# Performance work log

Hardware: AMD Instinct MI355X
Metric: run time of the kernel (lower is better)

Reference implementation:

```python
import jax, jax.numpy as jnp
import numpy as np

N_LAYERS = 2
D = 128


def _prelu(z, a):
    return jnp.where(z >= 0, z, a * z)


def _seg_sum(vals, idx, num):
    return jax.ops.segment_sum(vals, idx, num_segments=num)


def _conv_layer(x, ni, ei, Wn2e, bn2e, We2n, be2n, alpha, Dn_inv, De_inv, num_nodes, num_edges):
    # node -> edge: mean over member nodes (row norm), then linear + bias + PReLU
    e = _seg_sum((x @ Wn2e)[ni] * De_inv[ei][:, None], ei, num_edges) + bn2e
    e = _prelu(e, alpha)
    # edge -> node: mean over incident hyperedges
    n = _seg_sum((e @ We2n)[ei] * Dn_inv[ni][:, None], ni, num_nodes) + be2n
    return n, e


def _encoder(x, ni, ei, Wn2e, bn2e, We2n, be2n, alpha, Dn_inv, De_inv, num_nodes, num_edges):
    e = None
    for i in range(N_LAYERS):
        x, e = _conv_layer(x, ni, ei, Wn2e[i], bn2e[i], We2n[i], be2n[i], alpha, Dn_inv, De_inv, num_nodes, num_edges)
        x = _prelu(x, alpha)
    return x, e


def _decoder(x, e, ni, ei, We, Wx, b, alpha, Dn_inv, num_nodes):
    for i in range(N_LAYERS):
        m = _seg_sum((e @ We[i])[ei] * Dn_inv[ni][:, None], ni, num_nodes)
        x = _prelu(x @ Wx[i] + m + b[i], alpha)
    return x


def _forward(x, xx,
             e1_Wn2e, e1_bn2e, e1_We2n, e1_be2n,
             e2_Wn2e, e2_bn2e, e2_We2n, e2_be2n,
             d1_We, d1_Wx, d1_b, d2_We, d2_Wx, d2_b,
             alpha, node_idx, edge_idx, num_nodes, num_edges):
    # self loops: each node gets its own private hyperedge (id num_edges + node_id)
    ni = jnp.concatenate([node_idx, jnp.arange(num_nodes, dtype=node_idx.dtype)])
    ei = jnp.concatenate([edge_idx, jnp.arange(num_edges, num_edges + num_nodes, dtype=edge_idx.dtype)])
    ne_tot = num_edges + num_nodes
    ones = jnp.ones(ni.shape[0], x.dtype)
    Dn = _seg_sum(ones, ni, num_nodes)
    De = _seg_sum(ones, ei, ne_tot)
    Dn_inv = jnp.where(Dn > 0, 1.0 / Dn, 0.0)
    De_inv = jnp.where(De > 0, 1.0 / De, 0.0)

    n1, e1 = _encoder(x, ni, ei, e1_Wn2e, e1_bn2e, e1_We2n, e1_be2n, alpha, Dn_inv, De_inv, num_nodes, ne_tot)
    n2, e2 = _encoder(xx, ni, ei, e2_Wn2e, e2_bn2e, e2_We2n, e2_be2n, alpha, Dn_inv, De_inv, num_nodes, ne_tot)

    x11 = _decoder(n1, e1, ni, ei, d1_We, d1_Wx, d1_b, alpha, Dn_inv, num_nodes)
    x21 = _decoder(n2, e2, ni, ei, d2_We, d2_Wx, d2_b, alpha, Dn_inv, num_nodes)
    x12 = _decoder(n2, e2, ni, ei, d1_We, d1_Wx, d1_b, alpha, Dn_inv, num_nodes)
    x22 = _decoder(n1, e1, ni, ei, d2_We, d2_Wx, d2_b, alpha, Dn_inv, num_nodes)

    nn1 = jnp.concatenate([n1, n2], axis=1)
    return (nn1, n1, e1[:num_edges], n2, e2[:num_edges], x11, x21, x12, x22)


def setup_inputs() -> dict:
    key = jax.random.key(0)
    ks = jax.random.split(key, 24)
    N, E, NNZ = 50000, 20000, 800000
    s = 1.0 / np.sqrt(D)
    inp = {
        'x': jax.random.normal(ks[0], (N, D), jnp.float32),
        'xx': jax.random.normal(ks[1], (N, D), jnp.float32),
        'node_idx': jax.random.randint(ks[2], (NNZ,), 0, N, jnp.int32),
        'edge_idx': jax.random.randint(ks[3], (NNZ,), 0, E, jnp.int32),
        'num_nodes': N,
        'num_edges': E,
        'alpha': jnp.float32(0.25),
    }
    i = 4
    for enc in ('e1', 'e2'):
        inp[enc + '_Wn2e'] = jax.random.normal(ks[i], (N_LAYERS, D, D), jnp.float32) * s; i += 1
        inp[enc + '_bn2e'] = jnp.zeros((N_LAYERS, D), jnp.float32)
        inp[enc + '_We2n'] = jax.random.normal(ks[i], (N_LAYERS, D, D), jnp.float32) * s; i += 1
        inp[enc + '_be2n'] = jnp.zeros((N_LAYERS, D), jnp.float32)
    for dec in ('d1', 'd2'):
        inp[dec + '_We'] = jax.random.normal(ks[i], (N_LAYERS, D, D), jnp.float32) * s; i += 1
        inp[dec + '_Wx'] = jax.random.normal(ks[i], (N_LAYERS, D, D), jnp.float32) * s; i += 1
        inp[dec + '_b'] = jnp.zeros((N_LAYERS, D), jnp.float32)
    return inp


def reference(x, xx,
              e1_Wn2e, e1_bn2e, e1_We2n, e1_be2n,
              e2_Wn2e, e2_bn2e, e2_We2n, e2_be2n,
              d1_We, d1_Wx, d1_b, d2_We, d2_Wx, d2_b,
              alpha, node_idx, edge_idx, num_nodes, num_edges):
    return _forward(x, xx,
                    e1_Wn2e, e1_bn2e, e1_We2n, e1_be2n,
                    e2_Wn2e, e2_bn2e, e2_We2n, e2_be2n,
                    d1_We, d1_Wx, d1_b, d2_We, d2_Wx, d2_b,
                    alpha, node_idx, edge_idx, num_nodes, num_edges)
```

## Files before the change

### kernel.cpp

```cpp
#include <hip/hip_runtime.h>

#define DD 128

typedef __attribute__((ext_vector_type(8))) short bh8;
typedef __attribute__((ext_vector_type(8))) unsigned short us8;
typedef __attribute__((ext_vector_type(4))) unsigned short us4;
typedef __attribute__((ext_vector_type(4))) float f4;
typedef unsigned int u32;
typedef unsigned short u16;

__device__ __forceinline__ u16 tob(float f) {
  u32 u = __builtin_bit_cast(u32, f);
  u += 0x7FFFu + ((u >> 16) & 1u);
  return (u16)(u >> 16);
}
__device__ __forceinline__ float fb(u16 h) { return __builtin_bit_cast(float, (u32)h << 16); }


__global__ __launch_bounds__(256) void init_counts_k(int* cn, int* ce, int N, int E) {
  int g = blockIdx.x * blockDim.x + threadIdx.x;
  if (g < E) ce[g] = 0;
  if (g < N) cn[g] = 0;
}

__global__ __launch_bounds__(256) void hist_k(const int* __restrict__ ni, const int* __restrict__ ei,
                                              int* cn, int* ce, int nnz) {
  int stride = gridDim.x * blockDim.x;
  for (int j = blockIdx.x * blockDim.x + threadIdx.x; j < nnz; j += stride) {
    atomicAdd(&cn[ni[j]], 1);
    atomicAdd(&ce[ei[j]], 1);
  }
}

__global__ __launch_bounds__(1024) void exscan2_k(const int* __restrict__ cn, int* offs_n, int N,
                                                  const int* __restrict__ ce, int* offs_e, int E) {
  const int* cnt = blockIdx.x ? ce : cn;
  int* offs = blockIdx.x ? offs_e : offs_n;
  int n = blockIdx.x ? E : N;
  __shared__ int sums[1024];
  __shared__ int carry;
  const int tid = threadIdx.x;
  if (tid == 0) carry = 0;
  __syncthreads();
  const int PER = 8;
  const int CH = 1024 * PER;
  for (int base = 0; base < n; base += CH) {
    int i0 = base + tid * PER;
    int v[PER]; int s = 0;
    #pragma unroll
    for (int j = 0; j < PER; ++j) { int i = i0 + j; int t = (i < n) ? cnt[i] : 0; v[j] = t; s += t; }
    sums[tid] = s;
    __syncthreads();
    for (int off = 1; off < 1024; off <<= 1) {
      int t = (tid >= off) ? sums[tid - off] : 0;
      __syncthreads();
      sums[tid] += t;
      __syncthreads();
    }
    int excl = sums[tid] - s + carry;
    #pragma unroll
    for (int j = 0; j < PER; ++j) { int i = i0 + j; if (i < n) offs[i] = excl; excl += v[j]; }
    __syncthreads();
    if (tid == 0) carry += sums[1023];
    __syncthreads();
  }
  if (tid == 0) offs[n] = carry;
}

__global__ __launch_bounds__(256) void fill_deg_k(const int* __restrict__ offs_n, const int* __restrict__ offs_e,
                                                  float* Dn_inv, float* De_inv,
                                                  int* cur_be, int* cur_bn, int* cur_n, int* cur_e,
                                                  int N, int E, int NBE, int NBN) {
  int g = blockIdx.x * blockDim.x + threadIdx.x;
  if (g < E) {
    int b = offs_e[g], e = offs_e[g + 1];
    De_inv[g] = (e > b) ? 1.0f / (float)(e - b) : 0.0f;
    cur_e[g] = b;
  }
  if (g < N) {
    int b = offs_n[g], e = offs_n[g + 1];
    Dn_inv[g] = 1.0f / (float)(e - b + 1);
    cur_n[g] = b;
  }
  if (g < NBE) {
    int r1 = (g + 1) * 32; if (r1 > E) r1 = E;
    int o0 = offs_e[g * 32], o1 = offs_e[r1];
    int C = o1 - o0, base = 8 * o0;
    #pragma unroll
    for (int k = 0; k < 8; ++k) cur_be[g * 8 + k] = base + k * C;
  }
  if (g < NBN) {
    int r1 = (g + 1) * 32; if (r1 > N) r1 = N;
    int o0 = offs_n[g * 32], o1 = offs_n[r1];
    int C = o1 - o0, base = 8 * o0;
    #pragma unroll
    for (int k = 0; k < 8; ++k) cur_bn[g * 8 + k] = base + k * C;
  }
}

__global__ __launch_bounds__(256) void partition2_k(const int* __restrict__ ni, const int* __restrict__ ei,
                                                    int* cur_be, int* cur_bn,
                                                    u32* __restrict__ SE, u32* __restrict__ SN, int nnz) {
  int xcd;
  asm volatile("s_getreg_b32 %0, hwreg(HW_REG_XCC_ID)" : "=s"(xcd));
  xcd &= 7;
  int stride = gridDim.x * blockDim.x;
  for (int j = blockIdx.x * blockDim.x + threadIdx.x; j < nnz; j += stride) {
    int n = ni[j], e = ei[j];
    int pe = atomicAdd(&cur_be[(e >> 5) * 8 + xcd], 1);
    SE[pe] = ((u32)(e & 31) << 17) | (u32)n;
    int pn = atomicAdd(&cur_bn[(n >> 5) * 8 + xcd], 1);
    SN[pn] = ((u32)(n & 31) << 17) | (u32)e;
  }
}

__global__ __launch_bounds__(256) void scatter2_k(const u32* __restrict__ S, const int* __restrict__ offs,
                                                  const int* __restrict__ cur_b,
                                                  int* __restrict__ list, int nRows) {
  __shared__ int cur[32];
  const int b = blockIdx.x;
  const int i0 = b << 5;
  const int tid = threadIdx.x;
  if (tid < 32) {
    int row = i0 + tid;
    cur[tid] = (row < nRows) ? offs[row] : 0;
  }
  __syncthreads();
  int r1 = i0 + 32; if (r1 > nRows) r1 = nRows;
  const int o0 = offs[i0];
  const int C = offs[r1] - o0;
  #pragma unroll 1
  for (int k = 0; k < 8; ++k) {
    int sbeg = 8 * o0 + k * C;
    int send = cur_b[b * 8 + k];
    for (int i = sbeg + tid; i < send; i += 256) {
      u32 v = S[i];
      int pos = atomicAdd(&cur[v >> 17], 1);
      list[pos] = (int)(v & 0x1FFFFu);
    }
  }
}

__global__ __launch_bounds__(256) void fill_nnz_k(const int* __restrict__ ni, const int* __restrict__ ei,
                                                  int* cur_n, int* cur_e, int* listN, int* listE, int nnz) {
  int stride = gridDim.x * blockDim.x;
  for (int j = blockIdx.x * blockDim.x + threadIdx.x; j < nnz; j += stride) {
    int n = ni[j], e = ei[j];
    int pn = atomicAdd(&cur_n[n], 1); listN[pn] = e;
    int pe = atomicAdd(&cur_e[e], 1); listE[pe] = n;
  }
}


__device__ __forceinline__ void acc4(float4& a, us4 v) {
  a.x += fb(v[0]); a.y += fb(v[1]); a.z += fb(v[2]); a.w += fb(v[3]);
}

template<int SPLIT>
__global__ __launch_bounds__(256) void gather_edge_k(const u16* __restrict__ srcb,
                                                     const int* __restrict__ offs, const int* __restrict__ list,
                                                     const float* __restrict__ De_inv,
                                                     const float* __restrict__ b1, const float* __restrict__ b2,
                                                     const float* __restrict__ alphap,
                                                     u16* __restrict__ e_fullb,
                                                     float* __restrict__ d2a, float* __restrict__ d2b, int E) {
  const int wave = threadIdx.x >> 6, lane = threadIdx.x & 63;
  const int row = blockIdx.x * 4 + wave;
  if (row >= E) return;
  const int c = lane * 4;
  const int beg = offs[row], end = offs[row + 1];
  float4 a0 = {0,0,0,0}, a1 = {0,0,0,0}, a2 = {0,0,0,0}, a3 = {0,0,0,0};
  int i = beg;
  for (; i + 3 < end; i += 4) {
    int s0 = list[i], s1 = list[i + 1], s2 = list[i + 2], s3 = list[i + 3];
    us4 v0 = *(const us4*)&srcb[(size_t)s0 * 256 + c];
    us4 v1 = *(const us4*)&srcb[(size_t)s1 * 256 + c];
    us4 v2 = *(const us4*)&srcb[(size_t)s2 * 256 + c];
    us4 v3 = *(const us4*)&srcb[(size_t)s3 * 256 + c];
    acc4(a0, v0); acc4(a1, v1); acc4(a2, v2); acc4(a3, v3);
  }
  for (; i < end; ++i) acc4(a0, *(const us4*)&srcb[(size_t)list[i] * 256 + c]);
  float sc = De_inv[row];
  const float* bp = (c < 128) ? (b1 + c) : (b2 + c - 128);
  float4 bt = *(const float4*)bp;
  float al = *alphap;
  float4 o;
  o.x = sc * ((a0.x + a1.x) + (a2.x + a3.x)) + bt.x;
  o.y = sc * ((a0.y + a1.y) + (a2.y + a3.y)) + bt.y;
  o.z = sc * ((a0.z + a1.z) + (a2.z + a3.z)) + bt.z;
  o.w = sc * ((a0.w + a1.w) + (a2.w + a3.w)) + bt.w;
  o.x = (o.x >= 0.f) ? o.x : al * o.x;
  o.y = (o.y >= 0.f) ? o.y : al * o.y;
  o.z = (o.z >= 0.f) ? o.z : al * o.z;
  o.w = (o.w >= 0.f) ? o.w : al * o.w;
  us4 ob = {tob(o.x), tob(o.y), tob(o.z), tob(o.w)};
  *(us4*)&e_fullb[(size_t)row * 256 + c] = ob;
  if constexpr (SPLIT == 1) {
    if (c < 128) *(float4*)&d2a[(size_t)row * DD + c] = o;
    else         *(float4*)&d2b[(size_t)row * DD + c - 128] = o;
  }
}

__global__ __launch_bounds__(256) void gather_node_k(const u16* __restrict__ e_fullb,
                                                     const u16* __restrict__ tb,
                                                     const int* __restrict__ offs, const int* __restrict__ list,
                                                     const float* __restrict__ Dn_inv,
                                                     const float* __restrict__ b1, const float* __restrict__ b2,
                                                     const float* __restrict__ alphap,
                                                     u16* __restrict__ dstb, int N) {
  const int wave = threadIdx.x >> 6, lane = threadIdx.x & 63;
  const int row = blockIdx.x * 4 + wave;
  if (row >= N) return;
  const int c = lane * 4;
  const int beg = offs[row], end = offs[row + 1];
  float4 a0 = {0,0,0,0}, a1 = {0,0,0,0}, a2 = {0,0,0,0}, a3 = {0,0,0,0};
  int i = beg;
  for (; i + 3 < end; i += 4) {
    int s0 = list[i], s1 = list[i + 1], s2 = list[i + 2], s3 = list[i + 3];
    us4 v0 = *(const us4*)&e_fullb[(size_t)s0 * 256 + c];
    us4 v1 = *(const us4*)&e_fullb[(size_t)s1 * 256 + c];
    us4 v2 = *(const us4*)&e_fullb[(size_t)s2 * 256 + c];
    us4 v3 = *(const us4*)&e_fullb[(size_t)s3 * 256 + c];
    acc4(a0, v0); acc4(a1, v1); acc4(a2, v2); acc4(a3, v3);
  }
  for (; i < end; ++i) acc4(a0, *(const us4*)&e_fullb[(size_t)list[i] * 256 + c]);
  us4 tv4 = *(const us4*)&tb[(size_t)row * 256 + c];
  const float* bp = (c < 128) ? (b1 + c) : (b2 + c - 128);
  float4 bt = *(const float4*)bp;
  float al = *alphap;
  float sx = fb(tv4[0]) + bt.x; sx = (sx >= 0.f) ? sx : al * sx;
  float sy = fb(tv4[1]) + bt.y; sy = (sy >= 0.f) ? sy : al * sy;
  float sz = fb(tv4[2]) + bt.z; sz = (sz >= 0.f) ? sz : al * sz;
  float sw = fb(tv4[3]) + bt.w; sw = (sw >= 0.f) ? sw : al * sw;
  float sc = Dn_inv[row];
  us4 ob;
  ob[0] = tob(sc * (sx + ((a0.x + a1.x) + (a2.x + a3.x))));
  ob[1] = tob(sc * (sy + ((a0.y + a1.y) + (a2.y + a3.y))));
  ob[2] = tob(sc * (sz + ((a0.z + a1.z) + (a2.z + a3.z))));
  ob[3] = tob(sc * (sw + ((a0.w + a1.w) + (a2.w + a3.w))));
  *(us4*)&dstb[(size_t)row * 256 + c] = ob;
}


struct WPtrs { const float* p[16]; };

__global__ __launch_bounds__(256) void prep_w_k(WPtrs wp, char* dst) {
  int m = blockIdx.x >> 3, s = blockIdx.x & 7;
  const float* W = wp.p[m];
  int t = threadIdx.x;
  int n = t & 127;
  int k0 = s * 16 + (t >> 7) * 8;
  us8 vhi, vlo;
  #pragma unroll
  for (int j = 0; j < 8; ++j) {
    float x = W[(size_t)(k0 + j) * DD + n];
    u32 ux = __builtin_bit_cast(u32, x);
    float hf = __builtin_bit_cast(float, ux & 0xFFFF0000u);
    float l = x - hf;
    vhi[j] = (u16)(ux >> 16);
    vlo[j] = (u16)(__builtin_bit_cast(u32, l) >> 16);
  }
  char* base = dst + (size_t)m * 65536;
  int byte = n * 256 + k0 * 2;
  byte ^= (n & 7) << 4;
  *(us8*)(base + byte) = vhi;
  *(us8*)(base + 32768 + byte) = vlo;
}


__device__ __forceinline__ void stage_w(const char* gsrc, char* lds, int tid) {
  int wave = tid >> 6, lane = tid & 63;
  #pragma unroll
  for (int i = 0; i < 16; ++i) {
    int off = (wave * 16 + i) * 1024;
    __builtin_amdgcn_global_load_lds(
        (const __attribute__((address_space(1))) u32*)(gsrc + off + lane * 16),
        (__attribute__((address_space(3))) u32*)(lds + off), 16, 0, 0);
  }
}

__device__ __forceinline__ void split8(const float vs[8], bh8& hi, bh8& lo) {
  #pragma unroll
  for (int j = 0; j < 8; ++j) {
    u32 u = __builtin_bit_cast(u32, vs[j]);
    float hf = __builtin_bit_cast(float, u & 0xFFFF0000u);
    float l = vs[j] - hf;
    hi[j] = (short)(u >> 16);
    lo[j] = (short)(__builtin_bit_cast(u32, l) >> 16);
  }
}

__device__ __forceinline__ void mk_afrag(const float* rowp, int koff, bh8& hi, bh8& lo) {
  float4 v0 = *(const float4*)(rowp + koff);
  float4 v1 = *(const float4*)(rowp + koff + 4);
  float vs[8] = {v0.x, v0.y, v0.z, v0.w, v1.x, v1.y, v1.z, v1.w};
  split8(vs, hi, lo);
}

__device__ __forceinline__ void mfma_ks(const bh8& ahi, const bh8& alo, const char* Wl,
                                        int ks, int lane, f4 acc[8]) {
  const int koff0 = (lane >> 4) * 8;
  const int k2 = (ks * 32 + koff0) * 2;
  #pragma unroll
  for (int cb = 0; cb < 8; ++cb) {
    int n = cb * 16 + (lane & 15);
    int byte = (n * 256 + k2) ^ ((n & 7) << 4);
    bh8 bhiF = *(const bh8*)(Wl + byte);
    bh8 bloF = *(const bh8*)(Wl + 32768 + byte);
    acc[cb] = __builtin_amdgcn_mfma_f32_16x16x32_bf16(ahi, bhiF, acc[cb], 0, 0, 0);
    acc[cb] = __builtin_amdgcn_mfma_f32_16x16x32_bf16(ahi, bloF, acc[cb], 0, 0, 0);
    acc[cb] = __builtin_amdgcn_mfma_f32_16x16x32_bf16(alo, bhiF, acc[cb], 0, 0, 0);
  }
}

__device__ __forceinline__ void mfma_ks_bf(const bh8& a, const char* Wl,
                                           int ks, int lane, f4 acc[8]) {
  const int koff0 = (lane >> 4) * 8;
  const int k2 = (ks * 32 + koff0) * 2;
  #pragma unroll
  for (int cb = 0; cb < 8; ++cb) {
    int n = cb * 16 + (lane & 15);
    int byte = (n * 256 + k2) ^ ((n & 7) << 4);
    bh8 bhiF = *(const bh8*)(Wl + byte);
    bh8 bloF = *(const bh8*)(Wl + 32768 + byte);
    acc[cb] = __builtin_amdgcn_mfma_f32_16x16x32_bf16(a, bhiF, acc[cb], 0, 0, 0);
    acc[cb] = __builtin_amdgcn_mfma_f32_16x16x32_bf16(a, bloF, acc[cb], 0, 0, 0);
  }
}

__device__ __forceinline__ void mfma_passS(const float* __restrict__ A, size_t astride, int acoff,
                                           const char* Wl, int rbase, int nrows, int lane, f4 acc[8]) {
  int r = rbase + (lane & 15);
  if (r >= nrows) r = nrows - 1;
  const float* rowp = A + (size_t)r * astride + acoff;
  const int koff0 = (lane >> 4) * 8;
  #pragma unroll
  for (int ks = 0; ks < 4; ++ks) {
    bh8 ahi, alo;
    mk_afrag(rowp, ks * 32 + koff0, ahi, alo);
    mfma_ks(ahi, alo, Wl, ks, lane, acc);
  }
}

__device__ __forceinline__ void mfma_passB(const u16* __restrict__ A, size_t astride, int acoff,
                                           const char* Wl, int rbase, int nrows, int lane, f4 acc[8]) {
  int r = rbase + (lane & 15);
  if (r >= nrows) r = nrows - 1;
  const u16* rowp = A + (size_t)r * astride + acoff;
  const int koff0 = (lane >> 4) * 8;
  #pragma unroll
  for (int ks = 0; ks < 4; ++ks) {
    bh8 a = __builtin_bit_cast(bh8, *(const us8*)(rowp + ks * 32 + koff0));
    mfma_ks_bf(a, Wl, ks, lane, acc);
  }
}

struct AFragB { bh8 a[4]; };

__device__ __forceinline__ void load_afragB(const u16* __restrict__ A, size_t astride, int acoff,
                                            int rbase, int nrows, int lane, AFragB& f) {
  int r = rbase + (lane & 15);
  if (r >= nrows) r = nrows - 1;
  const u16* rowp = A + (size_t)r * astride + acoff;
  const int koff0 = (lane >> 4) * 8;
  #pragma unroll
  for (int ks = 0; ks < 4; ++ks)
    f.a[ks] = __builtin_bit_cast(bh8, *(const us8*)(rowp + ks * 32 + koff0));
}

__device__ __forceinline__ void mfma_pass_fragB(const AFragB& f, const char* Wl, int lane, f4 acc[8]) {
  #pragma unroll
  for (int ks = 0; ks < 4; ++ks) mfma_ks_bf(f.a[ks], Wl, ks, lane, acc);
}

template<int MODE, int OBF>
__device__ __forceinline__ void epilogueS(f4 acc[8], const float* bias, const float* alphap,
                                          void* outp, size_t ostride, int ocoff,
                                          int rbase, int nrows, int lane) {
  float al = 0.f;
  if constexpr (MODE == 1) al = *alphap;
  const int cidx = lane & 15;
  int rq = rbase + (lane >> 4) * 4;
  float b8[8];
  if constexpr (MODE == 1) {
    #pragma unroll
    for (int cb = 0; cb < 8; ++cb) b8[cb] = bias[cb * 16 + cidx];
  }
  #pragma unroll
  for (int q = 0; q < 4; ++q) {
    int row = rq + q;
    if (row < nrows) {
      #pragma unroll
      for (int cb = 0; cb < 8; ++cb) {
        float v = acc[cb][q];
        if constexpr (MODE == 1) { v += b8[cb]; v = (v >= 0.f) ? v : al * v; }
        if constexpr (OBF == 1) {
          u16* op = (u16*)outp + (size_t)row * ostride + ocoff + cidx;
          op[cb * 16] = tob(v);
        } else {
          float* op = (float*)outp + (size_t)row * ostride + ocoff + cidx;
          op[cb * 16] = v;
        }
      }
    }
  }
}

#define ACC_ZERO(acc) { _Pragma("unroll") for (int cb = 0; cb < 8; ++cb) acc[cb] = {0.f, 0.f, 0.f, 0.f}; }


template<int MODE, int OBF, int ABF>
__global__ __launch_bounds__(256, 2) void gemm_halves_k(const void* __restrict__ A1, size_t as1, int ac1, const char* W1, const float* b1_,
                                                        const void* __restrict__ A2, size_t as2, int ac2, const char* W2, const float* b2_,
                                                        const float* __restrict__ alphap,
                                                        void* __restrict__ out, int nrows) {
  __shared__ char Wl[65536];
  const int wave = threadIdx.x >> 6, lane = threadIdx.x & 63;
  const int rbase = blockIdx.x * 64 + wave * 16;
  f4 acc[8];
  stage_w(W1, Wl, threadIdx.x);
  __syncthreads();
  ACC_ZERO(acc);
  if constexpr (ABF) mfma_passB((const u16*)A1, as1, ac1, Wl, rbase, nrows, lane, acc);
  else               mfma_passS((const float*)A1, as1, ac1, Wl, rbase, nrows, lane, acc);
  epilogueS<MODE, OBF>(acc, b1_, alphap, out, 256, 0, rbase, nrows, lane);
  __syncthreads();
  stage_w(W2, Wl, threadIdx.x);
  __syncthreads();
  ACC_ZERO(acc);
  if constexpr (ABF) mfma_passB((const u16*)A2, as2, ac2, Wl, rbase, nrows, lane, acc);
  else               mfma_passS((const float*)A2, as2, ac2, Wl, rbase, nrows, lane, acc);
  epilogueS<MODE, OBF>(acc, b2_, alphap, out, 256, 128, rbase, nrows, lane);
}

__global__ __launch_bounds__(256, 2) void enc_final_k(const u16* __restrict__ aggb, const char* W1, const float* b1_,
                                                      const char* W2, const float* b2_,
                                                      const float* __restrict__ alphap,
                                                      float* __restrict__ n1, float* __restrict__ n2,
                                                      u16* __restrict__ n1b, u16* __restrict__ n2b,
                                                      float* __restrict__ nn1, int nrows) {
  __shared__ char Wl[65536];
  const int wave = threadIdx.x >> 6, lane = threadIdx.x & 63;
  const int rbase = blockIdx.x * 64 + wave * 16;
  const int cidx = lane & 15;
  f4 acc[8];
  float al = *alphap;
  #pragma unroll 1
  for (int h = 0; h < 2; ++h) {
    if (h) __syncthreads();
    stage_w(h ? W2 : W1, Wl, threadIdx.x);
    __syncthreads();
    const float* bp = h ? b2_ : b1_;
    float* nout = h ? n2 : n1;
    u16* nbout = h ? n2b : n1b;
    float b8[8];
    #pragma unroll
    for (int cb = 0; cb < 8; ++cb) b8[cb] = bp[cb * 16 + cidx];
    ACC_ZERO(acc);
    mfma_passB(aggb, 256, h * 128, Wl, rbase, nrows, lane, acc);
    int rq = rbase + (lane >> 4) * 4;
    #pragma unroll
    for (int q = 0; q < 4; ++q) {
      int row = rq + q;
      if (row < nrows) {
        float* op = nout + (size_t)row * DD + cidx;
        float* op2 = nn1 + (size_t)row * 256 + h * 128 + cidx;
        u16* op3 = nbout + (size_t)row * DD + cidx;
        #pragma unroll
        for (int cb = 0; cb < 8; ++cb) {
          float v = acc[cb][q] + b8[cb];
          v = (v >= 0.f) ? v : al * v;
          op[cb * 16] = v;
          op2[cb * 16] = v;
          op3[cb * 16] = tob(v);
        }
      }
    }
  }
}

template<int OBF>
__global__ __launch_bounds__(256, 2) void dec_pair2b_k(const u16* __restrict__ xA0, const u16* __restrict__ xB0,
                                                       const u16* __restrict__ xA1, const u16* __restrict__ xB1,
                                                       const u16* __restrict__ aggb,
                                                       const char* WxA, const char* WeA, const float* bA,
                                                       const char* WxB, const char* WeB, const float* bB,
                                                       const float* __restrict__ alphap,
                                                       void* __restrict__ o1_0, void* __restrict__ o2_0,
                                                       void* __restrict__ o1_1, void* __restrict__ o2_1,
                                                       int nrows) {
  __shared__ char Wl[65536];
  const int y = blockIdx.y;
  const u16* xA = y ? xA1 : xA0;
  const u16* xB = y ? xB1 : xB0;
  void* o1 = y ? o1_1 : o1_0;
  void* o2 = y ? o2_1 : o2_0;
  const int acoff = y * 128;
  const int wave = threadIdx.x >> 6, lane = threadIdx.x & 63;
  const int rbase = blockIdx.x * 64 + wave * 16;
  AFragB fa, fxA, fxB;
  load_afragB(aggb, 256, acoff, rbase, nrows, lane, fa);
  load_afragB(xA, DD, 0, rbase, nrows, lane, fxA);
  load_afragB(xB, DD, 0, rbase, nrows, lane, fxB);
  f4 acc[8];
  stage_w(WxA, Wl, threadIdx.x);
  __syncthreads();
  ACC_ZERO(acc);
  mfma_pass_fragB(fxA, Wl, lane, acc);
  __syncthreads();
  stage_w(WeA, Wl, threadIdx.x);
  __syncthreads();
  mfma_pass_fragB(fa, Wl, lane, acc);
  epilogueS<1, OBF>(acc, bA, alphap, o1, DD, 0, rbase, nrows, lane);
  __syncthreads();
  stage_w(WxB, Wl, threadIdx.x);
  __syncthreads();
  ACC_ZERO(acc);
  mfma_pass_fragB(fxB, Wl, lane, acc);
  __syncthreads();
  stage_w(WeB, Wl, threadIdx.x);
  __syncthreads();
  mfma_pass_fragB(fa, Wl, lane, acc);
  epilogueS<1, OBF>(acc, bB, alphap, o2, DD, 0, rbase, nrows, lane);
}


extern "C" void kernel_launch(void* const* d_in, const int* in_sizes, int n_in,
                              void* d_out, int out_size, void* d_ws, size_t ws_size,
                              hipStream_t stream) {
  const float* x        = (const float*)d_in[0];
  const float* xx       = (const float*)d_in[1];
  const int*   node_idx = (const int*)d_in[2];
  const int*   edge_idx = (const int*)d_in[3];
  const float* alphap   = (const float*)d_in[6];
  const float* e1_Wn2e  = (const float*)d_in[7];
  const float* e1_bn2e  = (const float*)d_in[8];
  const float* e1_We2n  = (const float*)d_in[9];
  const float* e1_be2n  = (const float*)d_in[10];
  const float* e2_Wn2e  = (const float*)d_in[11];
  const float* e2_bn2e  = (const float*)d_in[12];
  const float* e2_We2n  = (const float*)d_in[13];
  const float* e2_be2n  = (const float*)d_in[14];
  const float* d1_We    = (const float*)d_in[15];
  const float* d1_Wx    = (const float*)d_in[16];
  const float* d1_b     = (const float*)d_in[17];
  const float* d2_We    = (const float*)d_in[18];
  const float* d2_Wx    = (const float*)d_in[19];
  const float* d2_b     = (const float*)d_in[20];

  const int N   = in_sizes[0] / DD;
  const int NNZ = in_sizes[2];
  const int E   = (out_size - 1024 * N) / 256;
  const int NBE = (E + 31) >> 5;
  const int NBN = (N + 31) >> 5;

  float* out  = (float*)d_out;
  float* nn1  = out;
  float* n1   = out + (size_t)N * 256;
  float* e1o  = n1 + (size_t)N * DD;
  float* n2   = e1o + (size_t)E * DD;
  float* e2o  = n2 + (size_t)N * DD;
  float* x11  = e2o + (size_t)E * DD;
  float* x21  = x11 + (size_t)N * DD;
  float* x12  = x21 + (size_t)N * DD;
  float* x22  = x12 + (size_t)N * DD;

  size_t off = 0;
  char* w0 = (char*)d_ws;
  auto carve = [&](size_t bytes) -> void* {
    void* p = (void*)(w0 + off);
    off += (bytes + 255) & ~(size_t)255;
    return p;
  };
  int* cn      = (int*)carve((size_t)N * 4);
  int* ce      = (int*)carve((size_t)E * 4);
  int* offs_n  = (int*)carve((size_t)(N + 1) * 4);
  int* offs_e  = (int*)carve((size_t)(E + 1) * 4);
  int* listN   = (int*)carve((size_t)NNZ * 4);
  int* listE   = (int*)carve((size_t)NNZ * 4);
  float* Dn_inv = (float*)carve((size_t)N * 4);
  float* De_inv = (float*)carve((size_t)E * 4);
  char* Wprep  = (char*)carve((size_t)16 * 65536);
  u16* tb      = (u16*)carve((size_t)N * 256 * 2);
  u16* e_fullb = (u16*)carve((size_t)E * 256 * 2);
  u16* thb     = (u16*)carve((size_t)N * 256 * 2);
  u16* aggb    = (u16*)carve((size_t)N * 256 * 2);
  u16* t1b     = (u16*)carve((size_t)N * 256 * 2);
  u16* n1b     = (u16*)carve((size_t)N * DD * 2);
  u16* n2b     = (u16*)carve((size_t)N * DD * 2);
  u16* dt0a    = (u16*)carve((size_t)N * DD * 2);
  u16* dt1a    = (u16*)carve((size_t)N * DD * 2);
  u16* dt0b    = (u16*)carve((size_t)N * DD * 2);
  u16* dt1b    = (u16*)carve((size_t)N * DD * 2);
  int* cur_n   = (int*)carve((size_t)N * 4);
  int* cur_e   = (int*)carve((size_t)E * 4);
  int* cur_be  = (int*)carve((size_t)NBE * 8 * 4);
  int* cur_bn  = (int*)carve((size_t)NBN * 8 * 4);
  u32* SE      = (u32*)carve((size_t)NNZ * 8 * 4);
  u32* SN      = (u32*)carve((size_t)NNZ * 8 * 4);
  const bool staged = off <= ws_size;

  WPtrs wp;
  wp.p[0] = e1_Wn2e;  wp.p[1] = e1_Wn2e + DD * DD;
  wp.p[2] = e1_We2n;  wp.p[3] = e1_We2n + DD * DD;
  wp.p[4] = e2_Wn2e;  wp.p[5] = e2_Wn2e + DD * DD;
  wp.p[6] = e2_We2n;  wp.p[7] = e2_We2n + DD * DD;
  wp.p[8] = d1_We;    wp.p[9] = d1_We + DD * DD;
  wp.p[10] = d1_Wx;   wp.p[11] = d1_Wx + DD * DD;
  wp.p[12] = d2_We;   wp.p[13] = d2_We + DD * DD;
  wp.p[14] = d2_Wx;   wp.p[15] = d2_Wx + DD * DD;
  auto WP = [&](int i) -> const char* { return Wprep + (size_t)i * 65536; };

  const int thr = 256;
  const int gMax = ((N > E ? N : E) + thr - 1) / thr;
  int gNNZ = (NNZ + thr - 1) / thr; if (gNNZ > 2048) gNNZ = 2048;
  const int NT = (N + 63) / 64;
  const int gGatE = (E + 3) / 4;
  const int gGatN = (N + 3) / 4;

  prep_w_k<<<128, 256, 0, stream>>>(wp, Wprep);
  init_counts_k<<<gMax, thr, 0, stream>>>(cn, ce, N, E);
  hist_k<<<gNNZ, thr, 0, stream>>>(node_idx, edge_idx, cn, ce, NNZ);
  exscan2_k<<<2, 1024, 0, stream>>>(cn, offs_n, N, ce, offs_e, E);
  fill_deg_k<<<gMax, thr, 0, stream>>>(offs_n, offs_e, Dn_inv, De_inv,
                                       cur_be, cur_bn, cur_n, cur_e, N, E, NBE, NBN);

  if (staged) {
    partition2_k<<<gNNZ, thr, 0, stream>>>(node_idx, edge_idx, cur_be, cur_bn, SE, SN, NNZ);
    scatter2_k<<<NBE, 256, 0, stream>>>(SE, offs_e, cur_be, listE, E);
    scatter2_k<<<NBN, 256, 0, stream>>>(SN, offs_n, cur_bn, listN, N);
  } else {
    fill_nnz_k<<<gNNZ, thr, 0, stream>>>(node_idx, edge_idx, cur_n, cur_e, listN, listE, NNZ);
  }

  gemm_halves_k<0, 1, 0><<<NT, 256, 0, stream>>>(x, DD, 0, WP(0), nullptr,
                                                 xx, DD, 0, WP(4), nullptr, alphap, tb, N);
  gather_edge_k<0><<<gGatE, 256, 0, stream>>>(tb, offs_e, listE, De_inv, e1_bn2e, e2_bn2e,
                                              alphap, e_fullb, nullptr, nullptr, E);
  gather_node_k<<<gGatN, 256, 0, stream>>>(e_fullb, tb, offs_n, listN, Dn_inv, e1_bn2e, e2_bn2e,
                                           alphap, thb, N);
  gemm_halves_k<1, 1, 1><<<NT, 256, 0, stream>>>(thb, 256, 0, WP(2), e1_be2n,
                                                 thb, 256, 128, WP(6), e2_be2n, alphap, t1b, N);
  gemm_halves_k<0, 1, 1><<<NT, 256, 0, stream>>>(t1b, 256, 0, WP(1), nullptr,
                                                 t1b, 256, 128, WP(5), nullptr, alphap, tb, N);
  gather_edge_k<1><<<gGatE, 256, 0, stream>>>(tb, offs_e, listE, De_inv, e1_bn2e + DD, e2_bn2e + DD,
                                              alphap, e_fullb, e1o, e2o, E);
  gather_node_k<<<gGatN, 256, 0, stream>>>(e_fullb, tb, offs_n, listN, Dn_inv, e1_bn2e + DD, e2_bn2e + DD,
                                           alphap, aggb, N);
  enc_final_k<<<NT, 256, 0, stream>>>(aggb, WP(3), e1_be2n + DD, WP(7), e2_be2n + DD,
                                      alphap, n1, n2, n1b, n2b, nn1, N);

  dim3 gDec(NT, 2);
  dec_pair2b_k<1><<<gDec, 256, 0, stream>>>(n1b, n1b, n2b, n2b, aggb,
                                            WP(10), WP(8), d1_b, WP(14), WP(12), d2_b, alphap,
                                            dt0a, dt1a, dt0b, dt1b, N);
  dec_pair2b_k<0><<<gDec, 256, 0, stream>>>(dt0a, dt1a, dt0b, dt1b, aggb,
                                            WP(11), WP(9), d1_b + DD, WP(15), WP(13), d2_b + DD, alphap,
                                            x11, x22, x12, x21, N);
}
```

Baseline: 677.7 us.

## Parallelize degree scan and fuse chained GEMMs through LDS-staged intermediates

Replaces the two-block serial exclusive scan with a three-kernel multi-block scan (partials, chunk scan, apply) so the prefix sum runs across many workgroups. Fuses the two back-to-back encoder GEMM launches into one kernel that writes the PReLU'd bf16 intermediate into swizzled shared memory and feeds it straight into the second GEMM. Fuses the two decoder layers the same way, removing the t1b and dt* global intermediates and one launch each. The cost is more barriers and weight restaging per block, plus serialized work inside each fused kernel. The scan path also adds two extra launches and limits the chunk scan to 256 chunks.

Result: faster. 609.3 us (-10.1%).

```diff
diff --git a/kernel.cpp b/kernel.cpp
--- a/kernel.cpp
+++ b/kernel.cpp
@@ -32,39 +32,74 @@
   }
 }
 
-__global__ __launch_bounds__(1024) void exscan2_k(const int* __restrict__ cn, int* offs_n, int N,
-                                                  const int* __restrict__ ce, int* offs_e, int E) {
-  const int* cnt = blockIdx.x ? ce : cn;
-  int* offs = blockIdx.x ? offs_e : offs_n;
-  int n = blockIdx.x ? E : N;
-  __shared__ int sums[1024];
-  __shared__ int carry;
-  const int tid = threadIdx.x;
-  if (tid == 0) carry = 0;
+
+__global__ __launch_bounds__(256) void scan_partials_k(const int* __restrict__ cn, const int* __restrict__ ce,
+                                                       int* part, int NCHN, int N, int NCHE, int E) {
+  __shared__ int red[256];
+  int b = blockIdx.x, tid = threadIdx.x;
+  const int* cnt = (b < NCHN) ? cn : ce;
+  int n = (b < NCHN) ? N : E;
+  int base = ((b < NCHN) ? b : (b - NCHN)) << 10;
+  int i0 = base + tid * 4;
+  int s = 0;
+  #pragma unroll
+  for (int j = 0; j < 4; ++j) { int i = i0 + j; if (i < n) s += cnt[i]; }
+  red[tid] = s; __syncthreads();
+  for (int off = 128; off > 0; off >>= 1) {
+    if (tid < off) red[tid] += red[tid + off];
+    __syncthreads();
+  }
+  if (tid == 0) part[b] = red[0];
+}
+
+__device__ __forceinline__ int blk_excl_scan(int s, int tid, int* sums) {
+  sums[tid] = s; __syncthreads();
+  for (int off = 1; off < 256; off <<= 1) {
+    int t = (tid >= off) ? sums[tid - off] : 0;
+    __syncthreads();
+    sums[tid] += t;
+    __syncthreads();
+  }
+  int ex = sums[tid] - s;
   __syncthreads();
-  const int PER = 8;
-  const int CH = 1024 * PER;
-  for (int base = 0; base < n; base += CH) {
-    int i0 = base + tid * PER;
-    int v[PER]; int s = 0;
-    #pragma unroll
-    for (int j = 0; j < PER; ++j) { int i = i0 + j; int t = (i < n) ? cnt[i] : 0; v[j] = t; s += t; }
-    sums[tid] = s;
-    __syncthreads();
-    for (int off = 1; off < 1024; off <<= 1) {
-      int t = (tid >= off) ? sums[tid - off] : 0;
-      __syncthreads();
-      sums[tid] += t;
-      __syncthreads();
-    }
-    int excl = sums[tid] - s + carry;
-    #pragma unroll
-    for (int j = 0; j < PER; ++j) { int i = i0 + j; if (i < n) offs[i] = excl; excl += v[j]; }
-    __syncthreads();
-    if (tid == 0) carry += sums[1023];
-    __syncthreads();
-  }
-  if (tid == 0) offs[n] = carry;
+  return ex;
+}
+
+__global__ __launch_bounds__(256) void scan_chunks_k(int* part, int NCHN, int NCHE) {
+  __shared__ int sums[256];
+  int tid = threadIdx.x;
+  {
+    int v = (tid < NCHN) ? part[tid] : 0;
+    int ex = blk_excl_scan(v, tid, sums);
+    if (tid < NCHN) part[tid] = ex;
+  }
+  __syncthreads();
+  {
+    int v = (tid < NCHE) ? part[NCHN + tid] : 0;
+    int ex = blk_excl_scan(v, tid, sums);
+    if (tid < NCHE) part[NCHN + tid] = ex;
+  }
+}
+
+__global__ __launch_bounds__(256) void scan_apply_k(const int* __restrict__ cn, const int* __restrict__ ce,
+                                                    const int* __restrict__ part,
+                                                    int* offs_n, int* offs_e,
+                                                    int NCHN, int N, int NCHE, int E) {
+  __shared__ int sums[256];
+  int b = blockIdx.x, tid = threadIdx.x;
+  const int* cnt = (b < NCHN) ? cn : ce;
+  int* offs = (b < NCHN) ? offs_n : offs_e;
+  int n = (b < NCHN) ? N : E;
+  int base = ((b < NCHN) ? b : (b - NCHN)) << 10;
+  int i0 = base + tid * 4;
+  int v[4]; int s = 0;
+  #pragma unroll
+  for (int j = 0; j < 4; ++j) { int i = i0 + j; int t = (i < n) ? cnt[i] : 0; v[j] = t; s += t; }
+  int ex = blk_excl_scan(s, tid, sums);
+  int run = part[b] + ex;
+  #pragma unroll
+  for (int j = 0; j < 4; ++j) { int i = i0 + j; if (i < n) offs[i] = run; run += v[j]; }
+  if (tid == 255 && base + 1024 >= n) offs[n] = run;
 }
 
 __global__ __launch_bounds__(256) void fill_deg_k(const int* __restrict__ offs_n, const int* __restrict__ offs_e,
@@ -373,6 +408,36 @@
   for (int ks = 0; ks < 4; ++ks) mfma_ks_bf(f.a[ks], Wl, ks, lane, acc);
 }
 
+
+__device__ __forceinline__ void acc_to_T(f4 acc[8], const float* bias, float al,
+                                         char* Tb, int wave, int lane) {
+  const int cidx = lane & 15;
+  float b8[8];
+  #pragma unroll
+  for (int cb = 0; cb < 8; ++cb) b8[cb] = bias[cb * 16 + cidx];
+  #pragma unroll
+  for (int q = 0; q < 4; ++q) {
+    int row = wave * 16 + (lane >> 4) * 4 + q;
+    #pragma unroll
+    for (int cb = 0; cb < 8; ++cb) {
+      float v = acc[cb][q] + b8[cb];
+      v = (v >= 0.f) ? v : al * v;
+      int byte = (row * 256 + (cb * 16 + cidx) * 2) ^ ((row & 7) << 4);
+      *(u16*)(Tb + byte) = tob(v);
+    }
+  }
+}
+
+__device__ __forceinline__ void load_fT(const char* Tb, int wave, int lane, AFragB& f) {
+  const int row = wave * 16 + (lane & 15);
+  const int koff0 = (lane >> 4) * 8;
+  #pragma unroll
+  for (int ks = 0; ks < 4; ++ks) {
+    int byte = (row * 256 + (ks * 32 + koff0) * 2) ^ ((row & 7) << 4);
+    f.a[ks] = __builtin_bit_cast(bh8, *(const us8*)(Tb + byte));
+  }
+}
+
 template<int MODE, int OBF>
 __device__ __forceinline__ void epilogueS(f4 acc[8], const float* bias, const float* alphap,
                                           void* outp, size_t ostride, int ocoff,
@@ -431,6 +496,37 @@
   if constexpr (ABF) mfma_passB((const u16*)A2, as2, ac2, Wl, rbase, nrows, lane, acc);
   else               mfma_passS((const float*)A2, as2, ac2, Wl, rbase, nrows, lane, acc);
   epilogueS<MODE, OBF>(acc, b2_, alphap, out, 256, 128, rbase, nrows, lane);
+}
+
+__global__ __launch_bounds__(256, 2) void gemm_fuse_hid_k(const u16* __restrict__ thb,
+                                                          const char* W20, const float* b20, const char* W21,
+                                                          const char* W60, const float* b60, const char* W61,
+                                                          const float* __restrict__ alphap,
+                                                          u16* __restrict__ tb_out, int nrows) {
+  __shared__ char Wl[65536];
+  const int wave = threadIdx.x >> 6, lane = threadIdx.x & 63;
+  const int rbase = blockIdx.x * 64 + wave * 16;
+  const float al = *alphap;
+  f4 acc[8];
+  AFragB fT;
+  #pragma unroll 1
+  for (int h = 0; h < 2; ++h) {
+    if (h) __syncthreads();
+    stage_w(h ? W60 : W20, Wl, threadIdx.x);
+    __syncthreads();
+    ACC_ZERO(acc);
+    mfma_passB(thb, 256, h * 128, Wl, rbase, nrows, lane, acc);
+    __syncthreads();
+    acc_to_T(acc, h ? b60 : b20, al, Wl, wave, lane);
+    __syncthreads();
+    load_fT(Wl, wave, lane, fT);
+    __syncthreads();
+    stage_w(h ? W61 : W21, Wl, threadIdx.x);
+    __syncthreads();
+    ACC_ZERO(acc);
+    mfma_pass_fragB(fT, Wl, lane, acc);
+    epilogueS<0, 1>(acc, nullptr, nullptr, tb_out, 256, h * 128, rbase, nrows, lane);
+  }
 }
 
 __global__ __launch_bounds__(256, 2) void enc_final_k(const u16* __restrict__ aggb, const char* W1, const float* b1_,
@@ -479,49 +575,62 @@
   }
 }
 
-template<int OBF>
-__global__ __launch_bounds__(256, 2) void dec_pair2b_k(const u16* __restrict__ xA0, const u16* __restrict__ xB0,
-                                                       const u16* __restrict__ xA1, const u16* __restrict__ xB1,
-                                                       const u16* __restrict__ aggb,
-                                                       const char* WxA, const char* WeA, const float* bA,
-                                                       const char* WxB, const char* WeB, const float* bB,
-                                                       const float* __restrict__ alphap,
-                                                       void* __restrict__ o1_0, void* __restrict__ o2_0,
-                                                       void* __restrict__ o1_1, void* __restrict__ o2_1,
-                                                       int nrows) {
+__global__ __launch_bounds__(256, 2) void dec_fused_k(const u16* __restrict__ n1b, const u16* __restrict__ n2b,
+                                                      const u16* __restrict__ aggb,
+                                                      const char* Wx10, const char* We10, const float* b1_0,
+                                                      const char* Wx11, const char* We11, const float* b1_1,
+                                                      const char* Wx20, const char* We20, const float* b2_0,
+                                                      const char* Wx21, const char* We21, const float* b2_1,
+                                                      const float* __restrict__ alphap,
+                                                      float* __restrict__ x11, float* __restrict__ x22,
+                                                      float* __restrict__ x12, float* __restrict__ x21,
+                                                      int nrows) {
   __shared__ char Wl[65536];
   const int y = blockIdx.y;
-  const u16* xA = y ? xA1 : xA0;
-  const u16* xB = y ? xB1 : xB0;
-  void* o1 = y ? o1_1 : o1_0;
-  void* o2 = y ? o2_1 : o2_0;
+  const u16* xb = y ? n2b : n1b;
+  float* od1 = y ? x12 : x11;
+  float* od2 = y ? x21 : x22;
   const int acoff = y * 128;
   const int wave = threadIdx.x >> 6, lane = threadIdx.x & 63;
   const int rbase = blockIdx.x * 64 + wave * 16;
-  AFragB fa, fxA, fxB;
+  const float al = *alphap;
+  AFragB fx, fa, fT;
+  load_afragB(xb, DD, 0, rbase, nrows, lane, fx);
   load_afragB(aggb, 256, acoff, rbase, nrows, lane, fa);
-  load_afragB(xA, DD, 0, rbase, nrows, lane, fxA);
-  load_afragB(xB, DD, 0, rbase, nrows, lane, fxB);
   f4 acc[8];
-  stage_w(WxA, Wl, threadIdx.x);
-  __syncthreads();
-  ACC_ZERO(acc);
-  mfma_pass_fragB(fxA, Wl, lane, acc);
-  __syncthreads();
-  stage_w(WeA, Wl, threadIdx.x);
-  __syncthreads();
-  mfma_pass_fragB(fa, Wl, lane, acc);
-  epilogueS<1, OBF>(acc, bA, alphap, o1, DD, 0, rbase, nrows, lane);
-  __syncthreads();
-  stage_w(WxB, Wl, threadIdx.x);
-  __syncthreads();
-  ACC_ZERO(acc);
-  mfma_pass_fragB(fxB, Wl, lane, acc);
-  __syncthreads();
-  stage_w(WeB, Wl, threadIdx.x);
-  __syncthreads();
-  mfma_pass_fragB(fa, Wl, lane, acc);
-  epilogueS<1, OBF>(acc, bB, alphap, o2, DD, 0, rbase, nrows, lane);
+  #pragma unroll 1
+  for (int s = 0; s < 2; ++s) {
+    const char* Wx0 = s ? Wx20 : Wx10;
+    const char* We0 = s ? We20 : We10;
+    const char* Wx1 = s ? Wx21 : Wx11;
+    const char* We1 = s ? We21 : We11;
+    const float* b0 = s ? b2_0 : b1_0;
+    const float* b1 = s ? b2_1 : b1_1;
+    float* out = s ? od2 : od1;
+    if (s) __syncthreads();
+    stage_w(Wx0, Wl, threadIdx.x);
+    __syncthreads();
+    ACC_ZERO(acc);
+    mfma_pass_fragB(fx, Wl, lane, acc);
+    __syncthreads();
+    stage_w(We0, Wl, threadIdx.x);
+    __syncthreads();
+    mfma_pass_fragB(fa, Wl, lane, acc);
+    __syncthreads();
+    acc_to_T(acc, b0, al, Wl, wave, lane);
+    __syncthreads();
+    load_fT(Wl, wave, lane, fT);
+    __syncthreads();
+    stage_w(Wx1, Wl, threadIdx.x);
+    __syncthreads();
+    ACC_ZERO(acc);
+    mfma_pass_fragB(fT, Wl, lane, acc);
+    __syncthreads();
+    stage_w(We1, Wl, threadIdx.x);
+    __syncthreads();
+    mfma_pass_fragB(fa, Wl, lane, acc);
+    epilogueS<1, 0>(acc, b1, alphap, out, DD, 0, rbase, nrows, lane);
+  }
 }
 
 
@@ -553,6 +662,8 @@
   const int E   = (out_size - 1024 * N) / 256;
   const int NBE = (E + 31) >> 5;
   const int NBN = (N + 31) >> 5;
+  const int NCHN = (N + 1023) >> 10;
+  const int NCHE = (E + 1023) >> 10;
 
   float* out  = (float*)d_out;
   float* nn1  = out;
@@ -576,6 +687,7 @@
   int* ce      = (int*)carve((size_t)E * 4);
   int* offs_n  = (int*)carve((size_t)(N + 1) * 4);
   int* offs_e  = (int*)carve((size_t)(E + 1) * 4);
+  int* part    = (int*)carve((size_t)(NCHN + NCHE) * 4);
   int* listN   = (int*)carve((size_t)NNZ * 4);
   int* listE   = (int*)carve((size_t)NNZ * 4);
   float* Dn_inv = (float*)carve((size_t)N * 4);
@@ -585,13 +697,8 @@
   u16* e_fullb = (u16*)carve((size_t)E * 256 * 2);
   u16* thb     = (u16*)carve((size_t)N * 256 * 2);
   u16* aggb    = (u16*)carve((size_t)N * 256 * 2);
-  u16* t1b     = (u16*)carve((size_t)N * 256 * 2);
   u16* n1b     = (u16*)carve((size_t)N * DD * 2);
   u16* n2b     = (u16*)carve((size_t)N * DD * 2);
-  u16* dt0a    = (u16*)carve((size_t)N * DD * 2);
-  u16* dt1a    = (u16*)carve((size_t)N * DD * 2);
-  u16* dt0b    = (u16*)carve((size_t)N * DD * 2);
-  u16* dt1b    = (u16*)carve((size_t)N * DD * 2);
   int* cur_n   = (int*)carve((size_t)N * 4);
   int* cur_e   = (int*)carve((size_t)E * 4);
   int* cur_be  = (int*)carve((size_t)NBE * 8 * 4);
@@ -621,7 +728,9 @@
   prep_w_k<<<128, 256, 0, stream>>>(wp, Wprep);
   init_counts_k<<<gMax, thr, 0, stream>>>(cn, ce, N, E);
   hist_k<<<gNNZ, thr, 0, stream>>>(node_idx, edge_idx, cn, ce, NNZ);
-  exscan2_k<<<2, 1024, 0, stream>>>(cn, offs_n, N, ce, offs_e, E);
+  scan_partials_k<<<NCHN + NCHE, 256, 0, stream>>>(cn, ce, part, NCHN, N, NCHE, E);
+  scan_chunks_k<<<1, 256, 0, stream>>>(part, NCHN, NCHE);
+  scan_apply_k<<<NCHN + NCHE, 256, 0, stream>>>(cn, ce, part, offs_n, offs_e, NCHN, N, NCHE, E);
   fill_deg_k<<<gMax, thr, 0, stream>>>(offs_n, offs_e, Dn_inv, De_inv,
                                        cur_be, cur_bn, cur_n, cur_e, N, E, NBE, NBN);
 
@@ -639,10 +748,8 @@
                                               alphap, e_fullb, nullptr, nullptr, E);
   gather_node_k<<<gGatN, 256, 0, stream>>>(e_fullb, tb, offs_n, listN, Dn_inv, e1_bn2e, e2_bn2e,
                                            alphap, thb, N);
-  gemm_halves_k<1, 1, 1><<<NT, 256, 0, stream>>>(thb, 256, 0, WP(2), e1_be2n,
-                                                 thb, 256, 128, WP(6), e2_be2n, alphap, t1b, N);
-  gemm_halves_k<0, 1, 1><<<NT, 256, 0, stream>>>(t1b, 256, 0, WP(1), nullptr,
-                                                 t1b, 256, 128, WP(5), nullptr, alphap, tb, N);
+  gemm_fuse_hid_k<<<NT, 256, 0, stream>>>(thb, WP(2), e1_be2n, WP(1),
+                                          WP(6), e2_be2n, WP(5), alphap, tb, N);
   gather_edge_k<1><<<gGatE, 256, 0, stream>>>(tb, offs_e, listE, De_inv, e1_bn2e + DD, e2_bn2e + DD,
                                               alphap, e_fullb, e1o, e2o, E);
   gather_node_k<<<gGatN, 256, 0, stream>>>(e_fullb, tb, offs_n, listN, Dn_inv, e1_bn2e + DD, e2_bn2e + DD,
@@ -651,10 +758,8 @@
                                       alphap, n1, n2, n1b, n2b, nn1, N);
 
   dim3 gDec(NT, 2);
-  dec_pair2b_k<1><<<gDec, 256, 0, stream>>>(n1b, n1b, n2b, n2b, aggb,
-                                            WP(10), WP(8), d1_b, WP(14), WP(12), d2_b, alphap,
-                                            dt0a, dt1a, dt0b, dt1b, N);
-  dec_pair2b_k<0><<<gDec, 256, 0, stream>>>(dt0a, dt1a, dt0b, dt1b, aggb,
-                                            WP(11), WP(9), d1_b + DD, WP(15), WP(13), d2_b + DD, alphap,
-                                            x11, x22, x12, x21, N);
-}
+  dec_fused_k<<<gDec, 256, 0, stream>>>(n1b, n2b, aggb,
+                                        WP(10), WP(8), d1_b, WP(11), WP(9), d1_b + DD,
+                                        WP(14), WP(12), d2_b, WP(15), WP(13), d2_b + DD,
+                                        alphap, x11, x22, x12, x21, N);
+}
```
